# Kernel tuning notes

Hardware: AMD Instinct MI355X
Metric: run time of the kernel (lower is better)

Reference implementation:

```python
import jax, jax.numpy as jnp
import numpy as np


def setup_inputs() -> dict:
    key = jax.random.key(0)
    N, nH, D, L, P = 2, 8, 32, 4, 4
    shapes = np.array([[92, 92], [46, 46], [23, 23], [12, 12]], dtype=np.int64)
    areas = shapes[:, 0] * shapes[:, 1]
    Lin = int(areas.sum())  # 11253
    Lq = Lin  # encoder self-attention
    k1, k2, k3 = jax.random.split(key, 3)
    value = jax.random.normal(k1, (N, Lin, nH, D), dtype=jnp.float32)
    sampling_locations = jax.random.uniform(k2, (N, Lq, nH, L, P, 2), dtype=jnp.float32)
    aw = jax.random.uniform(k3, (N, Lq, nH, L, P), dtype=jnp.float32)
    attention_weights = aw / aw.sum(axis=(-2, -1), keepdims=True)  # softmax-normalized over L*P
    spatial_shapes = jnp.asarray(shapes)
    starts = np.concatenate([[0], np.cumsum(areas)[:-1]])
    level_start_index = jnp.asarray(starts, dtype=jnp.int64)
    return dict(value=value, spatial_shapes=spatial_shapes,
                level_start_index=level_start_index,
                sampling_locations=sampling_locations,
                attention_weights=attention_weights)


def _gather2d(v_nh, xi, yi, Hl, Wl):
    # v_nh: [N, nH, Hl*Wl, D]; xi, yi: [N, Lq, nH, P] int32 pixel coords
    N, Lq, nH, P = xi.shape
    valid = (xi >= 0) & (xi < Wl) & (yi >= 0) & (yi < Hl)
    xc = jnp.clip(xi, 0, Wl - 1)
    yc = jnp.clip(yi, 0, Hl - 1)
    idx = (yc * Wl + xc).transpose(0, 2, 1, 3).reshape(N, nH, Lq * P)
    vals = jax.vmap(jax.vmap(lambda v, i: v[i]))(v_nh, idx)  # [N, nH, Lq*P, D]
    vals = vals.reshape(N, nH, Lq, P, -1).transpose(0, 2, 1, 3, 4)  # [N, Lq, nH, P, D]
    return vals * valid[..., None].astype(vals.dtype)


def reference(value, spatial_shapes, level_start_index, sampling_locations, attention_weights):
    # ms_deform_attn core: per-level bilinear sampling (align_corners=False,
    # zero padding) at learned locations, weighted sum over levels and points.
    shapes_np = np.asarray(spatial_shapes)
    starts_np = np.asarray(level_start_index)
    N, Lin, nH, D = value.shape
    _, Lq, _, L, P, _ = sampling_locations.shape
    out = jnp.zeros((N, Lq, nH, D), dtype=value.dtype)
    for lvl in range(L):
        Hl, Wl = int(shapes_np[lvl, 0]), int(shapes_np[lvl, 1])
        s = int(starts_np[lvl])
        v_nh = value[:, s:s + Hl * Wl].transpose(0, 2, 1, 3)  # [N, nH, Hl*Wl, D]
        loc = sampling_locations[:, :, :, lvl]  # [N, Lq, nH, P, 2]
        # grid_sample convention: normalized [0,1] -> pixel coord, align_corners=False
        x = loc[..., 0] * Wl - 0.5
        y = loc[..., 1] * Hl - 0.5
        x0f = jnp.floor(x); y0f = jnp.floor(y)
        dx = x - x0f; dy = y - y0f
        x0 = x0f.astype(jnp.int32); y0 = y0f.astype(jnp.int32)
        x1 = x0 + 1; y1 = y0 + 1
        w00 = ((1.0 - dx) * (1.0 - dy))[..., None]
        w01 = (dx * (1.0 - dy))[..., None]
        w10 = ((1.0 - dx) * dy)[..., None]
        w11 = (dx * dy)[..., None]
        samp = (w00 * _gather2d(v_nh, x0, y0, Hl, Wl)
                + w01 * _gather2d(v_nh, x1, y0, Hl, Wl)
                + w10 * _gather2d(v_nh, x0, y1, Hl, Wl)
                + w11 * _gather2d(v_nh, x1, y1, Hl, Wl))  # [N, Lq, nH, P, D]
        aw_l = attention_weights[:, :, :, lvl]  # [N, Lq, nH, P]
        out = out + (samp * aw_l[..., None]).sum(axis=3)
    return out.reshape(N, Lq, nH * D)
```

## Files before the change

### kernel.cpp

```cpp
#include <hip/hip_runtime.h>

#define NH 8
#define DD 32
#define LL 4
#define PP 4

typedef float  f32x4  __attribute__((ext_vector_type(4)));
typedef float  f32x2  __attribute__((ext_vector_type(2)));
typedef int    i32x4  __attribute__((ext_vector_type(4)));
typedef _Float16 half4v __attribute__((ext_vector_type(4)));

__global__ __launch_bounds__(256) void conv_kernel(
    const float* __restrict__ value, _Float16* __restrict__ vh,
    int Lin, int total)
{
    int tid = blockIdx.x * blockDim.x + threadIdx.x;
    if (tid >= total) return;
    const int d4  = tid & 7;
    const int pos = (tid >> 3) % Lin;
    const int nh  = tid / (8 * Lin);
    const int n   = nh >> 3;
    const int h   = nh & 7;

    const f32x4 v = *(const f32x4*)(value + (((size_t)n * Lin + pos) * NH + h) * DD + d4 * 4);
    half4v o;
    o.x = (_Float16)v.x; o.y = (_Float16)v.y; o.z = (_Float16)v.z; o.w = (_Float16)v.w;
    *(half4v*)(vh + ((size_t)nh * Lin + pos) * DD + d4 * 4) = o;
}

#define FMAMIX_LO(ACC, DW, W) \
    asm("v_fma_mix_f32 %0, %1, %2, %0 op_sel:[0,0,0] op_sel_hi:[1,0,0]" \
        : "+v"(ACC) : "v"(DW), "v"(W))
#define FMAMIX_HI(ACC, DW, W) \
    asm("v_fma_mix_f32 %0, %1, %2, %0 op_sel:[1,0,0] op_sel_hi:[1,0,0]" \
        : "+v"(ACC) : "v"(DW), "v"(W))

__global__ __attribute__((amdgpu_flat_work_group_size(256, 256)))
__attribute__((amdgpu_waves_per_eu(4)))
void msda_fwd_h(
    const _Float16* __restrict__ vh,
    const int*   __restrict__ ssh,
    const int*   __restrict__ lsi,
    const float* __restrict__ sloc,
    const float* __restrict__ aw,
    float*       __restrict__ out,
    int N, int Lq, int Lin, int spx, int nSlabs)
{
    __shared__ i32x4 ent[32 * 41];

    const int xcd   = blockIdx.x & 7;
    const int blk   = blockIdx.x >> 3;
    const int sw    = blk % spx;
    const int chunk = blk / spx;
    const int slab  = xcd * spx + sw;
    if (slab >= nSlabs) return;

    const int t  = threadIdx.x;
    const int u  = t >> 3;
    const int j  = t & 7;
    const int q  = chunk * 32 + u;
    const int qc = min(q, Lq - 1);
    const int n  = slab >> 3;
    const int h  = slab & 7;

    {
        const size_t nqh = ((size_t)n * Lq + qc) * NH + h;
        const int l = j >> 1;
        const bool is64 = (ssh[1] == 0);
        const int W = is64 ? ssh[4 * l + 2] : ssh[2 * l + 1];
        const int H = is64 ? ssh[4 * l]     : ssh[2 * l];
        const int S = is64 ? lsi[2 * l]     : lsi[l];
        const f32x4 lc = __builtin_nontemporal_load((const f32x4*)sloc + nqh * 8 + j);
        const f32x2 av = __builtin_nontemporal_load((const f32x2*)aw + nqh * 8 + j);
        const float fW = (float)W, fH = (float)H;
        const int rowb  = W * (DD * 2);
        const int sbase = S * (DD * 2);
#pragma unroll
        for (int pt = 0; pt < 2; ++pt) {
            const float x  = lc[2 * pt]     * fW - 0.5f;
            const float y  = lc[2 * pt + 1] * fH - 0.5f;
            const float wq = av[pt];
            const float x0f = floorf(x), y0f = floorf(y);
            const int x0 = (int)x0f, y0 = (int)y0f;
            const float dx = x - x0f, dy = y - y0f;
            const int x1 = x0 + 1, y1 = y0 + 1;
            const bool vx0 = (x0 >= 0) & (x0 < W), vx1 = (x1 >= 0) & (x1 < W);
            const bool vy0 = (y0 >= 0) & (y0 < H), vy1 = (y1 >= 0) & (y1 < H);
            const int cx0 = min(max(x0, 0), W - 1), cx1 = min(max(x1, 0), W - 1);
            const int cy0 = min(max(y0, 0), H - 1), cy1 = min(max(y1, 0), H - 1);
            const float wx0 = (1.f - dx) * wq * (vx0 ? 1.f : 0.f);
            const float wx1 = dx         * wq * (vx1 ? 1.f : 0.f);
            const float ty  = (1.f - dy) * (vy0 ? 1.f : 0.f);
            const float by  = dy         * (vy1 ? 1.f : 0.f);
            const int rt = cy0 * rowb + sbase;
            const int rb = cy1 * rowb + sbase;
            i32x4 e0, e1;
            e0.x = rt + cx0 * (DD * 2);  e0.y = rb + cx0 * (DD * 2);
            e0.z = __float_as_int(wx0 * ty);  e0.w = __float_as_int(wx0 * by);
            e1.x = rt + cx1 * (DD * 2);  e1.y = rb + cx1 * (DD * 2);
            e1.z = __float_as_int(wx1 * ty);  e1.w = __float_as_int(wx1 * by);
            const int base = u * 41 + 5 * j + 2 * pt;
            ent[base]     = e0;
            ent[base + 1] = e1;
        }
    }
    __syncthreads();
    if (q >= Lq) return;

    const int side = j >> 2;
    const int cg   = j & 3;
    const char* __restrict__ sb =
        (const char*)vh + (size_t)slab * Lin * (DD * 2) + cg * 16;
    const int ub = u * 41 + side;

    float acc[8];
#pragma unroll
    for (int k = 0; k < 8; ++k) acc[k] = 0.f;

#define RD(b, E) { \
    E[0] = ent[ub + 10 * (b) + 0]; \
    E[1] = ent[ub + 10 * (b) + 2]; \
    E[2] = ent[ub + 10 * (b) + 5]; \
    E[3] = ent[ub + 10 * (b) + 7]; }
#define LD(E, V) _Pragma("unroll") \
    for (int i = 0; i < 4; ++i) { \
        V[2*i]   = *(const i32x4*)(sb + (unsigned)E[i].x); \
        V[2*i+1] = *(const i32x4*)(sb + (unsigned)E[i].y); }
#define AC(E, V) _Pragma("unroll") \
    for (int i = 0; i < 4; ++i) { \
        const float wt = __int_as_float(E[i].z); \
        const float wb = __int_as_float(E[i].w); \
        _Pragma("unroll") for (int d = 0; d < 4; ++d) { \
            FMAMIX_LO(acc[2*d],   V[2*i][d],   wt); \
            FMAMIX_HI(acc[2*d+1], V[2*i][d],   wt); \
            FMAMIX_LO(acc[2*d],   V[2*i+1][d], wb); \
            FMAMIX_HI(acc[2*d+1], V[2*i+1][d], wb); } }

    i32x4 E0[4], E1[4], E2[4], E3[4];
    i32x4 V0[8], V1[8], V2[8], V3[8];
    RD(0, E0) LD(E0, V0)
    RD(1, E1) LD(E1, V1)
    AC(E0, V0)
    RD(2, E2) LD(E2, V2)
    AC(E1, V1)
    RD(3, E3) LD(E3, V3)
    AC(E2, V2)
    AC(E3, V3)

#pragma unroll
    for (int k = 0; k < 8; ++k)
        acc[k] += __shfl_xor(acc[k], 4);

    f32x4 st;
    st.x = acc[side * 4 + 0];
    st.y = acc[side * 4 + 1];
    st.z = acc[side * 4 + 2];
    st.w = acc[side * 4 + 3];
    const size_t onqh = ((size_t)n * Lq + q) * NH + h;
    __builtin_nontemporal_store(st, (f32x4*)(out + onqh * DD + cg * 8 + side * 4));
}

__global__ __launch_bounds__(256) void msda_fwd_f32(
    const float* __restrict__ value,
    const int*   __restrict__ spatial_shapes,
    const int*   __restrict__ level_start,
    const float* __restrict__ sloc,
    const float* __restrict__ aw,
    float*       __restrict__ out,
    int N, int Lq, int Lin, int total)
{
    int tid = blockIdx.x * blockDim.x + threadIdx.x;
    if (tid >= total) return;
    const int c  = tid & 7;
    const int h  = (tid >> 3) & 7;
    const int nq = tid >> 6;
    const int n  = nq / Lq;
    const bool is64 = (spatial_shapes[1] == 0);
    int Hs[LL], Ws[LL], Ss[LL];
#pragma unroll
    for (int l = 0; l < LL; ++l) {
        if (is64) { Hs[l] = spatial_shapes[4*l]; Ws[l] = spatial_shapes[4*l+2]; Ss[l] = level_start[2*l]; }
        else      { Hs[l] = spatial_shapes[2*l]; Ws[l] = spatial_shapes[2*l+1]; Ss[l] = level_start[l]; }
    }
    const size_t nqh = (size_t)nq * NH + h;
    const float* loc_p = sloc + nqh * (LL * PP * 2);
    const float* aw_p  = aw   + nqh * (LL * PP);
    float4 acc = make_float4(0.f, 0.f, 0.f, 0.f);
#pragma unroll
    for (int l = 0; l < LL; ++l) {
        const int H = Hs[l], W = Ws[l];
        const float* vb = value + (((size_t)n * Lin + Ss[l]) * NH + h) * DD + c * 4;
#pragma unroll
        for (int p = 0; p < PP; ++p) {
            const int jj = l * PP + p;
            const float x = loc_p[2*jj] * (float)W - 0.5f;
            const float y = loc_p[2*jj+1] * (float)H - 0.5f;
            const float w = aw_p[jj];
            const float x0f = floorf(x), y0f = floorf(y);
            const int x0 = (int)x0f, y0 = (int)y0f, x1 = x0+1, y1 = y0+1;
            const float dx = x - x0f, dy = y - y0f;
            const bool vx0 = x0>=0 && x0<W, vx1 = x1>=0 && x1<W;
            const bool vy0 = y0>=0 && y0<H, vy1 = y1>=0 && y1<H;
            const int cx0 = min(max(x0,0),W-1), cx1 = min(max(x1,0),W-1);
            const int cy0 = min(max(y0,0),H-1), cy1 = min(max(y1,0),H-1);
            const float w00 = (1.f-dx)*(1.f-dy)*w*((vx0&&vy0)?1.f:0.f);
            const float w01 = dx*(1.f-dy)*w*((vx1&&vy0)?1.f:0.f);
            const float w10 = (1.f-dx)*dy*w*((vx0&&vy1)?1.f:0.f);
            const float w11 = dx*dy*w*((vx1&&vy1)?1.f:0.f);
            const float4 v00 = *(const float4*)(vb + (size_t)(cy0*W+cx0)*(NH*DD));
            const float4 v01 = *(const float4*)(vb + (size_t)(cy0*W+cx1)*(NH*DD));
            const float4 v10 = *(const float4*)(vb + (size_t)(cy1*W+cx0)*(NH*DD));
            const float4 v11 = *(const float4*)(vb + (size_t)(cy1*W+cx1)*(NH*DD));
            acc.x += w00*v00.x + w01*v01.x + w10*v10.x + w11*v11.x;
            acc.y += w00*v00.y + w01*v01.y + w10*v10.y + w11*v11.y;
            acc.z += w00*v00.z + w01*v01.z + w10*v10.z + w11*v11.z;
            acc.w += w00*v00.w + w01*v01.w + w10*v10.w + w11*v11.w;
        }
    }
    *(float4*)(out + nqh * DD + c * 4) = acc;
}

extern "C" void kernel_launch(void* const* d_in, const int* in_sizes, int n_in,
                              void* d_out, int out_size, void* d_ws, size_t ws_size,
                              hipStream_t stream)
{
    const float* value = (const float*)d_in[0];
    const int*   ss    = (const int*)  d_in[1];
    const int*   lsi   = (const int*)  d_in[2];
    const float* sloc  = (const float*)d_in[3];
    const float* aw    = (const float*)d_in[4];
    float* out = (float*)d_out;

    const int N = 2;
    const int Lq  = in_sizes[4] / (N * NH * LL * PP);
    const int Lin = in_sizes[0] / (N * NH * DD);

    const size_t need = (size_t)N * NH * Lin * DD * sizeof(_Float16);
    if (ws_size >= need) {
        _Float16* vh = (_Float16*)d_ws;
        const int ctotal = N * NH * Lin * 8;
        conv_kernel<<<(ctotal + 255) / 256, 256, 0, stream>>>(value, vh, Lin, ctotal);

        const int nSlabs = N * NH;
        const int spx    = (nSlabs + 7) / 8;
        const int chunks = (Lq + 31) / 32;
        const int grid   = 8 * spx * chunks;
        msda_fwd_h<<<grid, 256, 0, stream>>>(vh, ss, lsi, sloc, aw, out,
                                             N, Lq, Lin, spx, nSlabs);
    } else {
        const int total = N * Lq * NH * 8;
        msda_fwd_f32<<<(total + 255) / 256, 256, 0, stream>>>(value, ss, lsi, sloc, aw, out,
                                                              N, Lq, Lin, total);
    }
}
```

Baseline: 137.3 us.

## Map fp16 conversion blocks to same XCD as consumer slabs, raise occupancy

```diff
diff --git a/kernel.cpp b/kernel.cpp
--- a/kernel.cpp
+++ b/kernel.cpp
@@ -12,20 +12,26 @@
 
 __global__ __launch_bounds__(256) void conv_kernel(
     const float* __restrict__ value, _Float16* __restrict__ vh,
-    int Lin, int total)
-{
-    int tid = blockIdx.x * blockDim.x + threadIdx.x;
-    if (tid >= total) return;
-    const int d4  = tid & 7;
-    const int pos = (tid >> 3) % Lin;
-    const int nh  = tid / (8 * Lin);
-    const int n   = nh >> 3;
-    const int h   = nh & 7;
-
-    const f32x4 v = *(const f32x4*)(value + (((size_t)n * Lin + pos) * NH + h) * DD + d4 * 4);
+    int Lin, int spx, int nSlabs)
+{
+    const int xcd  = blockIdx.x & 7;
+    const int blk  = blockIdx.x >> 3;
+    const int sw   = blk % spx;
+    const int seg  = blk / spx;
+    const int slab = xcd * spx + sw;
+    if (slab >= nSlabs) return;
+    const int i = seg * 256 + threadIdx.x;
+    if (i >= Lin * 8) return;
+    const int d4  = i & 7;
+    const int pos = i >> 3;
+    const int n   = slab >> 3;
+    const int h   = slab & 7;
+
+    const f32x4 v = __builtin_nontemporal_load(
+        (const f32x4*)(value + (((size_t)n * Lin + pos) * NH + h) * DD + d4 * 4));
     half4v o;
     o.x = (_Float16)v.x; o.y = (_Float16)v.y; o.z = (_Float16)v.z; o.w = (_Float16)v.w;
-    *(half4v*)(vh + ((size_t)nh * Lin + pos) * DD + d4 * 4) = o;
+    *(half4v*)(vh + ((size_t)slab * Lin + pos) * DD + d4 * 4) = o;
 }
 
 #define FMAMIX_LO(ACC, DW, W) \
@@ -36,7 +42,7 @@
         : "+v"(ACC) : "v"(DW), "v"(W))
 
 __global__ __attribute__((amdgpu_flat_work_group_size(256, 256)))
-__attribute__((amdgpu_waves_per_eu(4)))
+__attribute__((amdgpu_waves_per_eu(8)))
 void msda_fwd_h(
     const _Float16* __restrict__ vh,
     const int*   __restrict__ ssh,
@@ -46,7 +52,7 @@
     float*       __restrict__ out,
     int N, int Lq, int Lin, int spx, int nSlabs)
 {
-    __shared__ i32x4 ent[32 * 41];
+    __shared__ i32x4 ent[32 * 39];
 
     const int xcd   = blockIdx.x & 7;
     const int blk   = blockIdx.x >> 3;
@@ -99,7 +105,7 @@
             e0.z = __float_as_int(wx0 * ty);  e0.w = __float_as_int(wx0 * by);
             e1.x = rt + cx1 * (DD * 2);  e1.y = rb + cx1 * (DD * 2);
             e1.z = __float_as_int(wx1 * ty);  e1.w = __float_as_int(wx1 * by);
-            const int base = u * 41 + 5 * j + 2 * pt;
+            const int base = u * 39 + 5 * j + 2 * pt;
             ent[base]     = e0;
             ent[base + 1] = e1;
         }
@@ -111,7 +117,7 @@
     const int cg   = j & 3;
     const char* __restrict__ sb =
         (const char*)vh + (size_t)slab * Lin * (DD * 2) + cg * 16;
-    const int ub = u * 41 + side;
+    const int ub = u * 39 + side;
 
     float acc[8];
 #pragma unroll
@@ -238,11 +244,11 @@
     const size_t need = (size_t)N * NH * Lin * DD * sizeof(_Float16);
     if (ws_size >= need) {
         _Float16* vh = (_Float16*)d_ws;
-        const int ctotal = N * NH * Lin * 8;
-        conv_kernel<<<(ctotal + 255) / 256, 256, 0, stream>>>(value, vh, Lin, ctotal);
-
         const int nSlabs = N * NH;
         const int spx    = (nSlabs + 7) / 8;
+        const int segs   = (Lin * 8 + 255) / 256;
+        conv_kernel<<<8 * spx * segs, 256, 0, stream>>>(value, vh, Lin, spx, nSlabs);
+
         const int chunks = (Lq + 31) / 32;
         const int grid   = 8 * spx * chunks;
         msda_fwd_h<<<grid, 256, 0, stream>>>(vh, ss, lsi, sloc, aw, out,
```

After: 144.1 us. 4.9% more time.

## Drop fp16 conversion pass and gather fp32 values directly in fused kernel

Applied to the files above, without the earlier changes.

```diff
diff --git a/kernel.cpp b/kernel.cpp
--- a/kernel.cpp
+++ b/kernel.cpp
@@ -8,50 +8,26 @@
 typedef float  f32x4  __attribute__((ext_vector_type(4)));
 typedef float  f32x2  __attribute__((ext_vector_type(2)));
 typedef int    i32x4  __attribute__((ext_vector_type(4)));
-typedef _Float16 half4v __attribute__((ext_vector_type(4)));
 
-__global__ __launch_bounds__(256) void conv_kernel(
-    const float* __restrict__ value, _Float16* __restrict__ vh,
-    int Lin, int total)
-{
-    int tid = blockIdx.x * blockDim.x + threadIdx.x;
-    if (tid >= total) return;
-    const int d4  = tid & 7;
-    const int pos = (tid >> 3) % Lin;
-    const int nh  = tid / (8 * Lin);
-    const int n   = nh >> 3;
-    const int h   = nh & 7;
-
-    const f32x4 v = *(const f32x4*)(value + (((size_t)n * Lin + pos) * NH + h) * DD + d4 * 4);
-    half4v o;
-    o.x = (_Float16)v.x; o.y = (_Float16)v.y; o.z = (_Float16)v.z; o.w = (_Float16)v.w;
-    *(half4v*)(vh + ((size_t)nh * Lin + pos) * DD + d4 * 4) = o;
-}
-
-#define FMAMIX_LO(ACC, DW, W) \
-    asm("v_fma_mix_f32 %0, %1, %2, %0 op_sel:[0,0,0] op_sel_hi:[1,0,0]" \
-        : "+v"(ACC) : "v"(DW), "v"(W))
-#define FMAMIX_HI(ACC, DW, W) \
-    asm("v_fma_mix_f32 %0, %1, %2, %0 op_sel:[1,0,0] op_sel_hi:[1,0,0]" \
-        : "+v"(ACC) : "v"(DW), "v"(W))
+#define SB() __builtin_amdgcn_sched_barrier(0)
 
 __global__ __attribute__((amdgpu_flat_work_group_size(256, 256)))
 __attribute__((amdgpu_waves_per_eu(4)))
-void msda_fwd_h(
-    const _Float16* __restrict__ vh,
+void msda_fwd_f(
+    const float* __restrict__ value,
     const int*   __restrict__ ssh,
     const int*   __restrict__ lsi,
     const float* __restrict__ sloc,
     const float* __restrict__ aw,
     float*       __restrict__ out,
-    int N, int Lq, int Lin, int spx, int nSlabs)
+    int N, int Lq, int Lin, int spx, int chunks, int nSlabs)
 {
-    __shared__ i32x4 ent[32 * 41];
+    __shared__ i32x4 ent[32 * 33];
 
     const int xcd   = blockIdx.x & 7;
     const int blk   = blockIdx.x >> 3;
-    const int sw    = blk % spx;
-    const int chunk = blk / spx;
+    const int sw    = blk / chunks;
+    const int chunk = blk % chunks;
     const int slab  = xcd * spx + sw;
     if (slab >= nSlabs) return;
 
@@ -73,8 +49,8 @@
         const f32x4 lc = __builtin_nontemporal_load((const f32x4*)sloc + nqh * 8 + j);
         const f32x2 av = __builtin_nontemporal_load((const f32x2*)aw + nqh * 8 + j);
         const float fW = (float)W, fH = (float)H;
-        const int rowb  = W * (DD * 2);
-        const int sbase = S * (DD * 2);
+        const int rowb = W * (NH * DD * 4);
+        const int sbase = S * (NH * DD * 4);
 #pragma unroll
         for (int pt = 0; pt < 2; ++pt) {
             const float x  = lc[2 * pt]     * fW - 0.5f;
@@ -94,130 +70,60 @@
             const float by  = dy         * (vy1 ? 1.f : 0.f);
             const int rt = cy0 * rowb + sbase;
             const int rb = cy1 * rowb + sbase;
-            i32x4 e0, e1;
-            e0.x = rt + cx0 * (DD * 2);  e0.y = rb + cx0 * (DD * 2);
-            e0.z = __float_as_int(wx0 * ty);  e0.w = __float_as_int(wx0 * by);
-            e1.x = rt + cx1 * (DD * 2);  e1.y = rb + cx1 * (DD * 2);
-            e1.z = __float_as_int(wx1 * ty);  e1.w = __float_as_int(wx1 * by);
-            const int base = u * 41 + 5 * j + 2 * pt;
-            ent[base]     = e0;
-            ent[base + 1] = e1;
+            const int o0 = cx0 * (NH * DD * 4), o1 = cx1 * (NH * DD * 4);
+            i32x4 et, eb;
+            et.x = rt + o0;  et.y = rt + o1;
+            et.z = __float_as_int(wx0 * ty);  et.w = __float_as_int(wx1 * ty);
+            eb.x = rb + o0;  eb.y = rb + o1;
+            eb.z = __float_as_int(wx0 * by);  eb.w = __float_as_int(wx1 * by);
+            const int p = 2 * j + pt;
+            ent[u * 33 + 2 * p]     = et;
+            ent[u * 33 + 2 * p + 1] = eb;
         }
     }
     __syncthreads();
     if (q >= Lq) return;
 
-    const int side = j >> 2;
-    const int cg   = j & 3;
     const char* __restrict__ sb =
-        (const char*)vh + (size_t)slab * Lin * (DD * 2) + cg * 16;
-    const int ub = u * 41 + side;
+        (const char*)value + (size_t)n * Lin * (NH * DD * 4) + h * (DD * 4) + j * 16;
+    const int ub = u * 33;
 
-    float acc[8];
-#pragma unroll
-    for (int k = 0; k < 8; ++k) acc[k] = 0.f;
+    f32x4 acc = {0.f, 0.f, 0.f, 0.f};
 
-#define RD(b, E) { \
-    E[0] = ent[ub + 10 * (b) + 0]; \
-    E[1] = ent[ub + 10 * (b) + 2]; \
-    E[2] = ent[ub + 10 * (b) + 5]; \
-    E[3] = ent[ub + 10 * (b) + 7]; }
-#define LD(E, V) _Pragma("unroll") \
+#define RD2(g, E) { \
+    E[0] = ent[ub + 4 * (g) + 0]; \
+    E[1] = ent[ub + 4 * (g) + 1]; \
+    E[2] = ent[ub + 4 * (g) + 2]; \
+    E[3] = ent[ub + 4 * (g) + 3]; }
+#define LD2(E, V) _Pragma("unroll") \
     for (int i = 0; i < 4; ++i) { \
-        V[2*i]   = *(const i32x4*)(sb + (unsigned)E[i].x); \
-        V[2*i+1] = *(const i32x4*)(sb + (unsigned)E[i].y); }
-#define AC(E, V) _Pragma("unroll") \
+        V[2*i]   = *(const f32x4*)(sb + (unsigned)E[i].x); \
+        V[2*i+1] = *(const f32x4*)(sb + (unsigned)E[i].y); }
+#define AC2(E, V) _Pragma("unroll") \
     for (int i = 0; i < 4; ++i) { \
-        const float wt = __int_as_float(E[i].z); \
-        const float wb = __int_as_float(E[i].w); \
+        const float wl = __int_as_float(E[i].z); \
+        const float wr = __int_as_float(E[i].w); \
         _Pragma("unroll") for (int d = 0; d < 4; ++d) { \
-            FMAMIX_LO(acc[2*d],   V[2*i][d],   wt); \
-            FMAMIX_HI(acc[2*d+1], V[2*i][d],   wt); \
-            FMAMIX_LO(acc[2*d],   V[2*i+1][d], wb); \
-            FMAMIX_HI(acc[2*d+1], V[2*i+1][d], wb); } }
+            acc[d] += wl * V[2*i][d]; \
+            acc[d] += wr * V[2*i+1][d]; } }
 
-    i32x4 E0[4], E1[4], E2[4], E3[4];
-    i32x4 V0[8], V1[8], V2[8], V3[8];
-    RD(0, E0) LD(E0, V0)
-    RD(1, E1) LD(E1, V1)
-    AC(E0, V0)
-    RD(2, E2) LD(E2, V2)
-    AC(E1, V1)
-    RD(3, E3) LD(E3, V3)
-    AC(E2, V2)
-    AC(E3, V3)
+    i32x4 EA[4], EB[4];
+    f32x4 V0[8], V1[8];
+    RD2(0, EA) RD2(1, EB)
+    SB();
+    LD2(EA, V0) LD2(EB, V1)
+    SB();
+    AC2(EA, V0) SB(); RD2(2, EA) SB(); LD2(EA, V0) SB();
+    AC2(EB, V1) SB(); RD2(3, EB) SB(); LD2(EB, V1) SB();
+    AC2(EA, V0) SB(); RD2(4, EA) SB(); LD2(EA, V0) SB();
+    AC2(EB, V1) SB(); RD2(5, EB) SB(); LD2(EB, V1) SB();
+    AC2(EA, V0) SB(); RD2(6, EA) SB(); LD2(EA, V0) SB();
+    AC2(EB, V1) SB(); RD2(7, EB) SB(); LD2(EB, V1) SB();
+    AC2(EA, V0)
+    AC2(EB, V1)
 
-#pragma unroll
-    for (int k = 0; k < 8; ++k)
-        acc[k] += __shfl_xor(acc[k], 4);
-
-    f32x4 st;
-    st.x = acc[side * 4 + 0];
-    st.y = acc[side * 4 + 1];
-    st.z = acc[side * 4 + 2];
-    st.w = acc[side * 4 + 3];
     const size_t onqh = ((size_t)n * Lq + q) * NH + h;
-    __builtin_nontemporal_store(st, (f32x4*)(out + onqh * DD + cg * 8 + side * 4));
-}
-
-__global__ __launch_bounds__(256) void msda_fwd_f32(
-    const float* __restrict__ value,
-    const int*   __restrict__ spatial_shapes,
-    const int*   __restrict__ level_start,
-    const float* __restrict__ sloc,
-    const float* __restrict__ aw,
-    float*       __restrict__ out,
-    int N, int Lq, int Lin, int total)
-{
-    int tid = blockIdx.x * blockDim.x + threadIdx.x;
-    if (tid >= total) return;
-    const int c  = tid & 7;
-    const int h  = (tid >> 3) & 7;
-    const int nq = tid >> 6;
-    const int n  = nq / Lq;
-    const bool is64 = (spatial_shapes[1] == 0);
-    int Hs[LL], Ws[LL], Ss[LL];
-#pragma unroll
-    for (int l = 0; l < LL; ++l) {
-        if (is64) { Hs[l] = spatial_shapes[4*l]; Ws[l] = spatial_shapes[4*l+2]; Ss[l] = level_start[2*l]; }
-        else      { Hs[l] = spatial_shapes[2*l]; Ws[l] = spatial_shapes[2*l+1]; Ss[l] = level_start[l]; }
-    }
-    const size_t nqh = (size_t)nq * NH + h;
-    const float* loc_p = sloc + nqh * (LL * PP * 2);
-    const float* aw_p  = aw   + nqh * (LL * PP);
-    float4 acc = make_float4(0.f, 0.f, 0.f, 0.f);
-#pragma unroll
-    for (int l = 0; l < LL; ++l) {
-        const int H = Hs[l], W = Ws[l];
-        const float* vb = value + (((size_t)n * Lin + Ss[l]) * NH + h) * DD + c * 4;
-#pragma unroll
-        for (int p = 0; p < PP; ++p) {
-            const int jj = l * PP + p;
-            const float x = loc_p[2*jj] * (float)W - 0.5f;
-            const float y = loc_p[2*jj+1] * (float)H - 0.5f;
-            const float w = aw_p[jj];
-            const float x0f = floorf(x), y0f = floorf(y);
-            const int x0 = (int)x0f, y0 = (int)y0f, x1 = x0+1, y1 = y0+1;
-            const float dx = x - x0f, dy = y - y0f;
-            const bool vx0 = x0>=0 && x0<W, vx1 = x1>=0 && x1<W;
-            const bool vy0 = y0>=0 && y0<H, vy1 = y1>=0 && y1<H;
-            const int cx0 = min(max(x0,0),W-1), cx1 = min(max(x1,0),W-1);
-            const int cy0 = min(max(y0,0),H-1), cy1 = min(max(y1,0),H-1);
-            const float w00 = (1.f-dx)*(1.f-dy)*w*((vx0&&vy0)?1.f:0.f);
-            const float w01 = dx*(1.f-dy)*w*((vx1&&vy0)?1.f:0.f);
-            const float w10 = (1.f-dx)*dy*w*((vx0&&vy1)?1.f:0.f);
-            const float w11 = dx*dy*w*((vx1&&vy1)?1.f:0.f);
-            const float4 v00 = *(const float4*)(vb + (size_t)(cy0*W+cx0)*(NH*DD));
-            const float4 v01 = *(const float4*)(vb + (size_t)(cy0*W+cx1)*(NH*DD));
-            const float4 v10 = *(const float4*)(vb + (size_t)(cy1*W+cx0)*(NH*DD));
-            const float4 v11 = *(const float4*)(vb + (size_t)(cy1*W+cx1)*(NH*DD));
-            acc.x += w00*v00.x + w01*v01.x + w10*v10.x + w11*v11.x;
-            acc.y += w00*v00.y + w01*v01.y + w10*v10.y + w11*v11.y;
-            acc.z += w00*v00.z + w01*v01.z + w10*v10.z + w11*v11.z;
-            acc.w += w00*v00.w + w01*v01.w + w10*v10.w + w11*v11.w;
-        }
-    }
-    *(float4*)(out + nqh * DD + c * 4) = acc;
+    __builtin_nontemporal_store(acc, (f32x4*)(out + onqh * DD + j * 4));
 }
 
 extern "C" void kernel_launch(void* const* d_in, const int* in_sizes, int n_in,
@@ -235,21 +141,10 @@
     const int Lq  = in_sizes[4] / (N * NH * LL * PP);
     const int Lin = in_sizes[0] / (N * NH * DD);
 
-    const size_t need = (size_t)N * NH * Lin * DD * sizeof(_Float16);
-    if (ws_size >= need) {
-        _Float16* vh = (_Float16*)d_ws;
-        const int ctotal = N * NH * Lin * 8;
-        conv_kernel<<<(ctotal + 255) / 256, 256, 0, stream>>>(value, vh, Lin, ctotal);
-
-        const int nSlabs = N * NH;
-        const int spx    = (nSlabs + 7) / 8;
-        const int chunks = (Lq + 31) / 32;
-        const int grid   = 8 * spx * chunks;
-        msda_fwd_h<<<grid, 256, 0, stream>>>(vh, ss, lsi, sloc, aw, out,
-                                             N, Lq, Lin, spx, nSlabs);
-    } else {
-        const int total = N * Lq * NH * 8;
-        msda_fwd_f32<<<(total + 255) / 256, 256, 0, stream>>>(value, ss, lsi, sloc, aw, out,
-                                                              N, Lq, Lin, total);
-    }
+    const int nSlabs = N * NH;
+    const int spx    = (nSlabs + 7) / 8;
+    const int chunks = (Lq + 31) / 32;
+    const int grid   = 8 * spx * chunks;
+    msda_fwd_f<<<grid, 256, 0, stream>>>(value, ss, lsi, sloc, aw, out,
+                                         N, Lq, Lin, spx, chunks, nSlabs);
 }
```

After: 261.3 us. 1.9x slower.
